# Optimization experiments

Measured on AMD Instinct MI355X. Metric: run time of the kernel, lower is better.

The kernel has to match this reference:

```python
import jax, jax.numpy as jnp
import numpy as np

T = 5       # Newton-Schulz iterations
EPS = 1e-5


def setup_inputs() -> dict:
    key = jax.random.key(0)
    k1, k2 = jax.random.split(key)
    N, F = 500000, 128
    X = jax.random.normal(k1, (N, F), dtype=jnp.float32)
    # running_rot buffer: random orthogonal rotation (eye at init; use QR for a non-trivial one)
    M = jax.random.normal(k2, (1, F, F), dtype=jnp.float32)
    Q, _ = jnp.linalg.qr(M)
    return {"X": X, "running_rot": Q.astype(jnp.float32)}


def _whiten(X):
    # iterative_normalization_py.forward, training path, g=1 group
    x = X.T[None]                              # [g=1, d, m]
    d, m = x.shape[1], x.shape[2]
    mean = jnp.mean(x, axis=-1, keepdims=True)
    xc = x - mean                              # centered [1, d, m]
    I = jnp.eye(d, dtype=X.dtype)[None]
    # Sigma = eps*I + xc xc^T / m  (baddbmm with beta=eps, alpha=1/m)
    Sigma = EPS * I + jnp.einsum('gdm,gem->gde', xc, xc) / m
    rTr = 1.0 / jnp.trace(Sigma, axis1=1, axis2=2)[:, None, None]  # 1/tr(Sigma)
    Sn = Sigma * rTr                           # trace-normalized covariance
    P = I
    for _ in range(T):                         # P_{k+1} = 1.5 P_k - 0.5 P_k^3 Sn
        P = 1.5 * P - 0.5 * (P @ P @ P @ Sn)
    wm = P * jnp.sqrt(rTr)                     # whitening matrix = Sigma^{-1/2} (approx)
    xn = wm @ xc                               # [1, d, m]
    return xn[0].T                             # back to [N, F]


def reference(X, running_rot):
    Xn = _whiten(X)                            # [N, F]
    # X_hat = einsum('bgc,gdc->bgd', X_hat, running_rot) with g=1
    out = jnp.einsum('nc,dc->nd', Xn, running_rot[0])
    return out
```

## Files before the change

### kernel.cpp

```cpp
#include <hip/hip_runtime.h>
#include <math.h>

#define NROWS  500000
#define NCHK   7813
#define EPSV   1e-5f

typedef __bf16 bf16_t;
typedef __bf16 bf16x4 __attribute__((ext_vector_type(4)));
typedef __bf16 bf16x8 __attribute__((ext_vector_type(8)));
typedef float  f32x4  __attribute__((ext_vector_type(4)));

static const size_t GT_OFF   = 131072;
static const size_t WB_OFF   = 327680;
static const size_t MEAN_OFF = 360448;
static const size_t BIAS_OFF = 360960;
static const size_t CS_OFF   = 393216;
static const size_t GRAM_OFF = 1048576;

__global__ __launch_bounds__(256) void k_stats(const float* __restrict__ X,
        float* __restrict__ csPart, float* __restrict__ gramPart) {
    __shared__ bf16_t sxtT[2][8192];
    __shared__ float  scs[256][4];
    const int t    = threadIdx.x;
    const int lane = t & 63;
    const int w    = t >> 6;
    const int oct  = t >> 5;
    const int fg4  = t & 31;
    const int cl   = lane & 15;
    const int kq   = lane >> 4;
    const int G    = gridDim.x;

    f32x4 acc[2][8];
    #pragma unroll
    for (int a = 0; a < 2; a++)
        #pragma unroll
        for (int b = 0; b < 8; b++)
            acc[a][b] = (f32x4){0.f, 0.f, 0.f, 0.f};
    float cs0 = 0.f, cs1 = 0.f, cs2 = 0.f, cs3 = 0.f;

    f32x4 R[8];

    auto KF = [](int f) { return (f ^ (f >> 3)) & 7; };

    auto GLOADC = [&](int ch) {
        const size_t row0 = (size_t)ch << 6;
        #pragma unroll
        for (int i = 0; i < 8; i++) {
            const size_t row = row0 + oct * 8 + i;
            R[i] = (row < NROWS)
                 ? *reinterpret_cast<const f32x4*>(X + row * 128 + fg4 * 4)
                 : (f32x4){0.f, 0.f, 0.f, 0.f};
        }
    };
    auto DSWRITEC = [&](int buf) {
        #pragma unroll
        for (int i = 0; i < 8; i++) {
            cs0 += R[i][0]; cs1 += R[i][1]; cs2 += R[i][2]; cs3 += R[i][3];
        }
        bf16_t* S = sxtT[buf];
        #pragma unroll
        for (int j = 0; j < 4; j++) {
            const int f = fg4 * 4 + j;
            const int g = oct ^ KF(f);
            bf16x8 v;
            #pragma unroll
            for (int i = 0; i < 8; i++) v[i] = (bf16_t)R[i][j];
            *reinterpret_cast<bf16x8*>(&S[f * 64 + g * 8]) = v;
        }
    };
    auto MFMAC = [&](int buf) {
        const bf16_t* S = sxtT[buf];
        #pragma unroll
        for (int kb = 0; kb < 2; kb++) {
            const int gq = kb * 4 + kq;
            bf16x8 fa[2];
            #pragma unroll
            for (int a = 0; a < 2; a++) {
                const int f = (w * 2 + a) * 16 + cl;
                fa[a] = *reinterpret_cast<const bf16x8*>(&S[f * 64 + ((gq ^ KF(f)) << 3)]);
            }
            #pragma unroll
            for (int b = 0; b < 8; b++) {
                const int f = b * 16 + cl;
                const bf16x8 fb = *reinterpret_cast<const bf16x8*>(&S[f * 64 + ((gq ^ KF(f)) << 3)]);
                acc[0][b] = __builtin_amdgcn_mfma_f32_16x16x32_bf16(fa[0], fb, acc[0][b], 0, 0, 0);
                acc[1][b] = __builtin_amdgcn_mfma_f32_16x16x32_bf16(fa[1], fb, acc[1][b], 0, 0, 0);
            }
        }
    };

    int ch0 = blockIdx.x;
    GLOADC(ch0);
    DSWRITEC(0);
    __syncthreads();
    for (;;) {
        const int ch1 = ch0 + G;
        const bool v1 = ch1 < NCHK;
        if (v1) GLOADC(ch1);
        MFMAC(0);
        if (v1) DSWRITEC(1);
        __syncthreads();
        if (!v1) break;
        const int ch2 = ch1 + G;
        const bool v2 = ch2 < NCHK;
        if (v2) GLOADC(ch2);
        MFMAC(1);
        if (v2) DSWRITEC(0);
        __syncthreads();
        if (!v2) break;
        ch0 = ch2;
    }

    float* gp = gramPart + (size_t)blockIdx.x * 16384;
    #pragma unroll
    for (int a = 0; a < 2; a++)
        #pragma unroll
        for (int b = 0; b < 8; b++)
            #pragma unroll
            for (int r = 0; r < 4; r++) {
                const int row = (w * 2 + a) * 16 + kq * 4 + r;
                const int col = b * 16 + cl;
                gp[row * 128 + col] = acc[a][b][r];
            }
    scs[t][0] = cs0; scs[t][1] = cs1; scs[t][2] = cs2; scs[t][3] = cs3;
    __syncthreads();
    if (t < 128) {
        float s = 0.f;
        #pragma unroll
        for (int q = 0; q < 8; q++) s += scs[q * 32 + (t >> 2)][t & 3];
        csPart[(size_t)blockIdx.x * 128 + t] = s;
    }
}

__global__ __launch_bounds__(256) void k_gred(const float* __restrict__ gramPart,
        const float* __restrict__ csPart, float* __restrict__ gramTot,
        float* __restrict__ mean, int G) {
    const int t = threadIdx.x;
    const int b = blockIdx.x;
    if (b == 256) {
        if (t < 128) {
            float s = 0.f;
            int g = 0;
            for (; g + 8 <= G; g += 8) {
                float p[8];
                #pragma unroll
                for (int u = 0; u < 8; u++) p[u] = csPart[(size_t)(g + u) * 128 + t];
                s += ((p[0] + p[1]) + (p[2] + p[3])) + ((p[4] + p[5]) + (p[6] + p[7]));
            }
            for (; g < G; g++) s += csPart[(size_t)g * 128 + t];
            mean[t] = s * (1.0f / (float)NROWS);
        }
        return;
    }
    const int e  = b * 64 + (t & 63);
    const int sl = t >> 6;
    float s = 0.f;
    int g = sl;
    for (; g + 28 < G; g += 32) {
        float v[8];
        #pragma unroll
        for (int u = 0; u < 8; u++)
            v[u] = gramPart[(size_t)(g + 4 * u) * 16384 + e];
        s += ((v[0] + v[1]) + (v[2] + v[3])) + ((v[4] + v[5]) + (v[6] + v[7]));
    }
    for (; g < G; g += 4)
        s += gramPart[(size_t)g * 16384 + e];
    __shared__ float red[4][64];
    red[sl][t & 63] = s;
    __syncthreads();
    if (t < 64)
        gramTot[b * 64 + t] = (red[0][t] + red[1][t]) + (red[2][t] + red[3][t]);
}

__global__ __launch_bounds__(256) void k_ns(const float* __restrict__ gramTot,
        const float* __restrict__ mean, const float* __restrict__ Rg,
        bf16_t* __restrict__ Wb, float* __restrict__ bias) {
    __shared__ bf16_t sPh[16384], sPl[16384], sSn[16384], sTT[16384];
    const int t = threadIdx.x;
    const int w = t >> 6, lane = t & 63;
    const int cl = lane & 15, kq = lane >> 4;

    float* rs = reinterpret_cast<float*>(sTT);
    float dv = 0.f;
    if (t < 128) {
        const float m = mean[t];
        dv = gramTot[t * 129] * (1.0f / (float)NROWS) - m * m + EPSV;
    }
    rs[t] = dv;
    __syncthreads();
    #pragma unroll
    for (int off = 128; off > 0; off >>= 1) {
        if (t < off) rs[t] += rs[t + off];
        __syncthreads();
    }
    const float rTr = 1.0f / rs[0];
    __syncthreads();
    for (int i = 0; i < 64; i++) {
        const int e = t + (i << 8);
        const int r = e >> 7, c = e & 127;
        float s = gramTot[e] * (1.0f / (float)NROWS) - mean[r] * mean[c];
        if (r == c) s += EPSV;
        const int ix = r * 128 + (c ^ ((r & 7) << 3));
        const float snv = s * rTr;
        sSn[ix] = (bf16_t)snv;
        const float p0 = ((r == c) ? 1.5f : 0.f) - 0.5f * snv;
        const bf16_t ph = (bf16_t)p0;
        sPh[ix] = ph;
        sPl[ix] = (bf16_t)(p0 - (float)ph);
    }
    __syncthreads();

    f32x4 acc[2][8];
    auto NSMM = [&](const bf16_t* __restrict__ Bm) {
        #pragma unroll
        for (int a = 0; a < 2; a++)
            #pragma unroll
            for (int ct = 0; ct < 8; ct++) acc[a][ct] = (f32x4){0.f, 0.f, 0.f, 0.f};
        #pragma unroll
        for (int kb = 0; kb < 4; kb++) {
            const int k0 = kb * 32 + kq * 8;
            bf16x8 ah[2], al[2];
            #pragma unroll
            for (int a = 0; a < 2; a++) {
                const int ra = w * 32 + a * 16 + cl;
                const int ia = ra * 128 + (k0 ^ ((ra & 7) << 3));
                ah[a] = *reinterpret_cast<const bf16x8*>(&sPh[ia]);
                al[a] = *reinterpret_cast<const bf16x8*>(&sPl[ia]);
            }
            #pragma unroll
            for (int ct = 0; ct < 8; ct++) {
                const int rb = ct * 16 + cl;
                const bf16x8 bb = *reinterpret_cast<const bf16x8*>(
                    &Bm[rb * 128 + (k0 ^ ((rb & 7) << 3))]);
                acc[0][ct] = __builtin_amdgcn_mfma_f32_16x16x32_bf16(ah[0], bb, acc[0][ct], 0, 0, 0);
                acc[0][ct] = __builtin_amdgcn_mfma_f32_16x16x32_bf16(al[0], bb, acc[0][ct], 0, 0, 0);
                acc[1][ct] = __builtin_amdgcn_mfma_f32_16x16x32_bf16(ah[1], bb, acc[1][ct], 0, 0, 0);
                acc[1][ct] = __builtin_amdgcn_mfma_f32_16x16x32_bf16(al[1], bb, acc[1][ct], 0, 0, 0);
            }
        }
    };
    auto WRT = [&](bf16_t* __restrict__ D) {
        #pragma unroll
        for (int a = 0; a < 2; a++) {
            const int ro0 = w * 32 + a * 16 + kq * 4;
            #pragma unroll
            for (int ct = 0; ct < 8; ct++) {
                const int co = ct * 16 + cl;
                bf16x4 v = { (bf16_t)acc[a][ct][0], (bf16_t)acc[a][ct][1],
                             (bf16_t)acc[a][ct][2], (bf16_t)acc[a][ct][3] };
                *reinterpret_cast<bf16x4*>(&D[co * 128 + (ro0 ^ ((co & 7) << 3))]) = v;
            }
        }
    };

    for (int it = 0; it < 4; it++) {
        NSMM(sSn);
        WRT(sTT);
        __syncthreads();
        NSMM(sTT);
        __syncthreads();
        WRT(sTT);
        __syncthreads();
        NSMM(sTT);
        #pragma unroll
        for (int a = 0; a < 2; a++) {
            const int ro0 = w * 32 + a * 16 + kq * 4;
            #pragma unroll
            for (int ct = 0; ct < 8; ct++) {
                const int co = ct * 16 + cl;
                const int ix = co * 128 + (ro0 ^ ((co & 7) << 3));
                bf16x4 ph4 = *reinterpret_cast<const bf16x4*>(&sPh[ix]);
                bf16x4 pl4 = *reinterpret_cast<const bf16x4*>(&sPl[ix]);
                bf16x4 nh, nl;
                #pragma unroll
                for (int r = 0; r < 4; r++) {
                    const float pold = (float)ph4[r] + (float)pl4[r];
                    const float pn = 1.5f * pold - 0.5f * acc[a][ct][r];
                    nh[r] = (bf16_t)pn;
                    nl[r] = (bf16_t)(pn - (float)nh[r]);
                }
                *reinterpret_cast<bf16x4*>(&sPh[ix]) = nh;
                *reinterpret_cast<bf16x4*>(&sPl[ix]) = nl;
            }
        }
        __syncthreads();
    }

    const float scal = sqrtf(rTr);
    #pragma unroll
    for (int a = 0; a < 2; a++)
        #pragma unroll
        for (int ct = 0; ct < 8; ct++) acc[a][ct] = (f32x4){0.f, 0.f, 0.f, 0.f};
    #pragma unroll
    for (int kb = 0; kb < 4; kb++) {
        const int k0 = kb * 32 + kq * 8;
        bf16x8 ah[2], al[2];
        #pragma unroll
        for (int a = 0; a < 2; a++) {
            const int ra = w * 32 + a * 16 + cl;
            const float4 rv0 = *reinterpret_cast<const float4*>(&Rg[ra * 128 + k0]);
            const float4 rv1 = *reinterpret_cast<const float4*>(&Rg[ra * 128 + k0 + 4]);
            const float rv[8] = {rv0.x, rv0.y, rv0.z, rv0.w, rv1.x, rv1.y, rv1.z, rv1.w};
            bf16x8 h, l;
            #pragma unroll
            for (int j = 0; j < 8; j++) {
                h[j] = (bf16_t)rv[j];
                l[j] = (bf16_t)(rv[j] - (float)h[j]);
            }
            ah[a] = h; al[a] = l;
        }
        #pragma unroll
        for (int ct = 0; ct < 8; ct++) {
            const int rb = ct * 16 + cl;
            const int ib = rb * 128 + (k0 ^ ((rb & 7) << 3));
            const bf16x8 bh = *reinterpret_cast<const bf16x8*>(&sPh[ib]);
            const bf16x8 bl = *reinterpret_cast<const bf16x8*>(&sPl[ib]);
            #pragma unroll
            for (int a = 0; a < 2; a++) {
                acc[a][ct] = __builtin_amdgcn_mfma_f32_16x16x32_bf16(ah[a], bh, acc[a][ct], 0, 0, 0);
                acc[a][ct] = __builtin_amdgcn_mfma_f32_16x16x32_bf16(al[a], bh, acc[a][ct], 0, 0, 0);
                acc[a][ct] = __builtin_amdgcn_mfma_f32_16x16x32_bf16(ah[a], bl, acc[a][ct], 0, 0, 0);
            }
        }
    }
    #pragma unroll
    for (int a = 0; a < 2; a++) {
        float pb[4] = {0.f, 0.f, 0.f, 0.f};
        #pragma unroll
        for (int ct = 0; ct < 8; ct++) {
            const float mv = mean[ct * 16 + cl];
            #pragma unroll
            for (int r = 0; r < 4; r++) {
                const float wv = acc[a][ct][r] * scal;
                Wb[(w * 32 + a * 16 + kq * 4 + r) * 128 + ct * 16 + cl] = (bf16_t)wv;
                pb[r] += wv * mv;
            }
        }
        #pragma unroll
        for (int r = 0; r < 4; r++) {
            float v = pb[r];
            v += __shfl_xor(v, 1);
            v += __shfl_xor(v, 2);
            v += __shfl_xor(v, 4);
            v += __shfl_xor(v, 8);
            if (cl == 0) bias[w * 32 + a * 16 + kq * 4 + r] = v;
        }
    }
}

__global__ __launch_bounds__(256) void k_out(const float* __restrict__ X,
        const bf16_t* __restrict__ Wb, const float* __restrict__ bias,
        float* __restrict__ out) {
    __shared__ bf16_t sW[128][136];
    __shared__ float sBias[128];
    const int t = threadIdx.x;
    const int w = t >> 6, lane = t & 63;
    const int cl = lane & 15, kq = lane >> 4;
    const int tile = NCHK - 1 - blockIdx.x;
    const size_t rowbase = (size_t)tile * 64 + (size_t)w * 16;
    const bool valid = rowbase < NROWS;

    float4 B[8];
    {
        const float* xr = X + (rowbase + cl) * 128;
        #pragma unroll
        for (int kb = 0; kb < 4; kb++) {
            B[2*kb]   = valid ? *reinterpret_cast<const float4*>(xr + kb*32 + kq*8)
                              : float4{0.f,0.f,0.f,0.f};
            B[2*kb+1] = valid ? *reinterpret_cast<const float4*>(xr + kb*32 + kq*8 + 4)
                              : float4{0.f,0.f,0.f,0.f};
        }
    }
    #pragma unroll
    for (int i = 0; i < 8; i++) {
        const int idx = (t + (i << 8)) << 3;
        *reinterpret_cast<bf16x8*>(&sW[idx >> 7][idx & 127]) =
            *reinterpret_cast<const bf16x8*>(&Wb[idx]);
    }
    if (t < 128) sBias[t] = bias[t];
    __syncthreads();
    if (!valid) return;

    bf16x8 xh[4], xl[4];
    #pragma unroll
    for (int kb = 0; kb < 4; kb++) {
        const float4 v0 = B[2*kb], v1 = B[2*kb+1];
        const float xv[8] = {v0.x, v0.y, v0.z, v0.w, v1.x, v1.y, v1.z, v1.w};
        bf16x8 h, l;
        #pragma unroll
        for (int j = 0; j < 8; j++) {
            h[j] = (bf16_t)xv[j];
            l[j] = (bf16_t)(xv[j] - (float)h[j]);
        }
        xh[kb] = h; xl[kb] = l;
    }
    float* orow = out + (rowbase + cl) * 128;
    #pragma unroll
    for (int ct = 0; ct < 8; ct++) {
        f32x4 acc = (f32x4){0.f, 0.f, 0.f, 0.f};
        const int d = ct * 16 + cl;
        #pragma unroll
        for (int kb = 0; kb < 4; kb++) {
            const bf16x8 wf = *reinterpret_cast<const bf16x8*>(&sW[d][kb*32 + kq*8]);
            acc = __builtin_amdgcn_mfma_f32_16x16x32_bf16(wf, xl[kb], acc, 0, 0, 0);
            acc = __builtin_amdgcn_mfma_f32_16x16x32_bf16(wf, xh[kb], acc, 0, 0, 0);
        }
        const f32x4 bv = *reinterpret_cast<const f32x4*>(&sBias[ct * 16 + kq * 4]);
        const f32x4 o = acc - bv;
        __builtin_nontemporal_store(o,
            reinterpret_cast<f32x4*>(&orow[ct * 16 + kq * 4]));
    }
}

extern "C" void kernel_launch(void* const* d_in, const int* in_sizes, int n_in,
                              void* d_out, int out_size, void* d_ws, size_t ws_size,
                              hipStream_t stream) {
    const float* X = (const float*)d_in[0];
    const float* R = (const float*)d_in[1];
    float* out = (float*)d_out;
    char* ws = (char*)d_ws;
    float*  gramTot = (float*)(ws + GT_OFF);
    bf16_t* Wb      = (bf16_t*)(ws + WB_OFF);
    float*  mean    = (float*)(ws + MEAN_OFF);
    float*  bias    = (float*)(ws + BIAS_OFF);
    float*  csPart  = (float*)(ws + CS_OFF);

    int G = 512;
    size_t avail = (ws_size > GRAM_OFF) ? (ws_size - GRAM_OFF) : 0;
    if (avail < (size_t)G * 65536) {
        G = (int)(avail / 65536);
        if (G < 1) G = 1;
        if (G > 512) G = 512;
    }
    float* gramPart = (float*)(ws + GRAM_OFF);

    k_stats<<<dim3(G), dim3(256), 0, stream>>>(X, csPart, gramPart);
    k_gred<<<dim3(257), dim3(256), 0, stream>>>(gramPart, csPart, gramTot, mean, G);
    k_ns<<<dim3(1), dim3(256), 0, stream>>>(gramTot, mean, R, Wb, bias);
    k_out<<<dim3(NCHK), dim3(256), 0, stream>>>(X, Wb, bias, out);
}
```

Measured before the change: 210.3 us.

## Make output kernel persistent with register double-buffered X prefetch, vectorize gram stores

The output projection kernel now runs on a fixed grid of 1024 blocks that loop over row tiles. Each block keeps two register buffers so it can load the next X tile while running MFMA on the current one, and the one-time staging of the weights and bias into shared memory is amortized across tiles. The stats kernel now writes each per-block Gram partial as transposed, vectorized nontemporal float4 stores; this is valid because each partial is symmetric. The reduction kernel reads those partials with nontemporal loads. In exchange, the prefetch buffers and the launch-bounds occupancy hint raise register pressure, and fewer blocks in flight could reduce latency hiding.

Measured after the change: 199.6 us. 1.05x faster.

```diff
diff --git a/kernel.cpp b/kernel.cpp
--- a/kernel.cpp
+++ b/kernel.cpp
@@ -115,13 +115,12 @@
     #pragma unroll
     for (int a = 0; a < 2; a++)
         #pragma unroll
-        for (int b = 0; b < 8; b++)
-            #pragma unroll
-            for (int r = 0; r < 4; r++) {
-                const int row = (w * 2 + a) * 16 + kq * 4 + r;
-                const int col = b * 16 + cl;
-                gp[row * 128 + col] = acc[a][b][r];
-            }
+        for (int b = 0; b < 8; b++) {
+            const int col  = b * 16 + cl;
+            const int row0 = (w * 2 + a) * 16 + kq * 4;
+            __builtin_nontemporal_store(acc[a][b],
+                reinterpret_cast<f32x4*>(&gp[col * 128 + row0]));
+        }
     scs[t][0] = cs0; scs[t][1] = cs1; scs[t][2] = cs2; scs[t][3] = cs3;
     __syncthreads();
     if (t < 128) {
@@ -160,11 +159,11 @@
         float v[8];
         #pragma unroll
         for (int u = 0; u < 8; u++)
-            v[u] = gramPart[(size_t)(g + 4 * u) * 16384 + e];
+            v[u] = __builtin_nontemporal_load(&gramPart[(size_t)(g + 4 * u) * 16384 + e]);
         s += ((v[0] + v[1]) + (v[2] + v[3])) + ((v[4] + v[5]) + (v[6] + v[7]));
     }
     for (; g < G; g += 4)
-        s += gramPart[(size_t)g * 16384 + e];
+        s += __builtin_nontemporal_load(&gramPart[(size_t)g * 16384 + e]);
     __shared__ float red[4][64];
     red[sl][t & 63] = s;
     __syncthreads();
@@ -348,7 +347,7 @@
     }
 }
 
-__global__ __launch_bounds__(256) void k_out(const float* __restrict__ X,
+__global__ __launch_bounds__(256, 4) void k_out(const float* __restrict__ X,
         const bf16_t* __restrict__ Wb, const float* __restrict__ bias,
         float* __restrict__ out) {
     __shared__ bf16_t sW[128][136];
@@ -356,21 +355,58 @@
     const int t = threadIdx.x;
     const int w = t >> 6, lane = t & 63;
     const int cl = lane & 15, kq = lane >> 4;
-    const int tile = NCHK - 1 - blockIdx.x;
-    const size_t rowbase = (size_t)tile * 64 + (size_t)w * 16;
-    const bool valid = rowbase < NROWS;
-
-    float4 B[8];
-    {
-        const float* xr = X + (rowbase + cl) * 128;
+    const int G = gridDim.x;
+
+    float4 A0[8], A1[8];
+
+    auto GLOAD = [&](int tl, float4 (&B)[8]) {
+        const size_t rowb = (size_t)tl * 64 + (size_t)w * 16;
+        const bool v = rowb < NROWS;
+        const float* xr = X + (rowb + cl) * 128;
         #pragma unroll
         for (int kb = 0; kb < 4; kb++) {
-            B[2*kb]   = valid ? *reinterpret_cast<const float4*>(xr + kb*32 + kq*8)
-                              : float4{0.f,0.f,0.f,0.f};
-            B[2*kb+1] = valid ? *reinterpret_cast<const float4*>(xr + kb*32 + kq*8 + 4)
-                              : float4{0.f,0.f,0.f,0.f};
-        }
-    }
+            B[2*kb]   = v ? *reinterpret_cast<const float4*>(xr + kb*32 + kq*8)
+                          : float4{0.f,0.f,0.f,0.f};
+            B[2*kb+1] = v ? *reinterpret_cast<const float4*>(xr + kb*32 + kq*8 + 4)
+                          : float4{0.f,0.f,0.f,0.f};
+        }
+    };
+    auto COMPSTORE = [&](int tl, const float4 (&B)[8]) {
+        const size_t rowbase = (size_t)tl * 64 + (size_t)w * 16;
+        if (rowbase >= NROWS) return;
+        bf16x8 xh[4], xl[4];
+        #pragma unroll
+        for (int kb = 0; kb < 4; kb++) {
+            const float4 v0 = B[2*kb], v1 = B[2*kb+1];
+            const float xv[8] = {v0.x, v0.y, v0.z, v0.w, v1.x, v1.y, v1.z, v1.w};
+            bf16x8 h, l;
+            #pragma unroll
+            for (int j = 0; j < 8; j++) {
+                h[j] = (bf16_t)xv[j];
+                l[j] = (bf16_t)(xv[j] - (float)h[j]);
+            }
+            xh[kb] = h; xl[kb] = l;
+        }
+        float* orow = out + (rowbase + cl) * 128;
+        #pragma unroll
+        for (int ct = 0; ct < 8; ct++) {
+            f32x4 acc = (f32x4){0.f, 0.f, 0.f, 0.f};
+            const int d = ct * 16 + cl;
+            #pragma unroll
+            for (int kb = 0; kb < 4; kb++) {
+                const bf16x8 wf = *reinterpret_cast<const bf16x8*>(&sW[d][kb*32 + kq*8]);
+                acc = __builtin_amdgcn_mfma_f32_16x16x32_bf16(wf, xl[kb], acc, 0, 0, 0);
+                acc = __builtin_amdgcn_mfma_f32_16x16x32_bf16(wf, xh[kb], acc, 0, 0, 0);
+            }
+            const f32x4 bv = *reinterpret_cast<const f32x4*>(&sBias[ct * 16 + kq * 4]);
+            const f32x4 o = acc - bv;
+            __builtin_nontemporal_store(o,
+                reinterpret_cast<f32x4*>(&orow[ct * 16 + kq * 4]));
+        }
+    };
+
+    int t0 = blockIdx.x;
+    GLOAD(t0, A0);
     #pragma unroll
     for (int i = 0; i < 8; i++) {
         const int idx = (t + (i << 8)) << 3;
@@ -379,36 +415,16 @@
     }
     if (t < 128) sBias[t] = bias[t];
     __syncthreads();
-    if (!valid) return;
-
-    bf16x8 xh[4], xl[4];
-    #pragma unroll
-    for (int kb = 0; kb < 4; kb++) {
-        const float4 v0 = B[2*kb], v1 = B[2*kb+1];
-        const float xv[8] = {v0.x, v0.y, v0.z, v0.w, v1.x, v1.y, v1.z, v1.w};
-        bf16x8 h, l;
-        #pragma unroll
-        for (int j = 0; j < 8; j++) {
-            h[j] = (bf16_t)xv[j];
-            l[j] = (bf16_t)(xv[j] - (float)h[j]);
-        }
-        xh[kb] = h; xl[kb] = l;
-    }
-    float* orow = out + (rowbase + cl) * 128;
-    #pragma unroll
-    for (int ct = 0; ct < 8; ct++) {
-        f32x4 acc = (f32x4){0.f, 0.f, 0.f, 0.f};
-        const int d = ct * 16 + cl;
-        #pragma unroll
-        for (int kb = 0; kb < 4; kb++) {
-            const bf16x8 wf = *reinterpret_cast<const bf16x8*>(&sW[d][kb*32 + kq*8]);
-            acc = __builtin_amdgcn_mfma_f32_16x16x32_bf16(wf, xl[kb], acc, 0, 0, 0);
-            acc = __builtin_amdgcn_mfma_f32_16x16x32_bf16(wf, xh[kb], acc, 0, 0, 0);
-        }
-        const f32x4 bv = *reinterpret_cast<const f32x4*>(&sBias[ct * 16 + kq * 4]);
-        const f32x4 o = acc - bv;
-        __builtin_nontemporal_store(o,
-            reinterpret_cast<f32x4*>(&orow[ct * 16 + kq * 4]));
+    for (;;) {
+        const int t1 = t0 + G;
+        if (t1 < NCHK) GLOAD(t1, A1);
+        COMPSTORE(t0, A0);
+        if (t1 >= NCHK) break;
+        const int t2 = t1 + G;
+        if (t2 < NCHK) GLOAD(t2, A0);
+        COMPSTORE(t1, A1);
+        if (t2 >= NCHK) break;
+        t0 = t2;
     }
 }
 
@@ -437,5 +453,5 @@
     k_stats<<<dim3(G), dim3(256), 0, stream>>>(X, csPart, gramPart);
     k_gred<<<dim3(257), dim3(256), 0, stream>>>(gramPart, csPart, gramTot, mean, G);
     k_ns<<<dim3(1), dim3(256), 0, stream>>>(gramTot, mean, R, Wb, bias);
-    k_out<<<dim3(NCHK), dim3(256), 0, stream>>>(X, Wb, bias, out);
+    k_out<<<dim3(1024), dim3(256), 0, stream>>>(X, Wb, bias, out);
 }
```
